# Optimization experiments

Measured on AMD Instinct MI355X. Metric: run time of the kernel, lower is better.

## Reference

```python
import jax, jax.numpy as jnp
import numpy as np

K = 3          # kernel_size
STRIDE = 1
BLOCK = 64     # block_size
OUT_FEATURES = 512
IN_CH = 256
IN_FEATURES = K * K * IN_CH          # 2304
Q = IN_FEATURES // BLOCK             # 36 (exact)
P = OUT_FEATURES // BLOCK            # 8


def _unfold(x, k, stride):
    # torch F.unfold with padding=k//2: output (B, C*k*k, Ho*Wo),
    # feature order channel-major then (di, dj)
    B, C, H, W = x.shape
    pad = k // 2
    xp = jnp.pad(x, ((0, 0), (0, 0), (pad, pad), (pad, pad)))
    Ho = (H + 2 * pad - k) // stride + 1
    Wo = (W + 2 * pad - k) // stride + 1
    cols = jnp.stack(
        [xp[:, :, di:di + (Ho - 1) * stride + 1:stride,
                  dj:dj + (Wo - 1) * stride + 1:stride]
         for di in range(k) for dj in range(k)],
        axis=2)  # (B, C, k*k, Ho, Wo)
    return cols.reshape(B, C * k * k, Ho * Wo), Ho, Wo


def setup_inputs() -> dict:
    key = jax.random.key(0)
    k1, k2 = jax.random.split(key)
    x = jax.random.normal(k1, (8, IN_CH, 32, 32), dtype=jnp.float32)
    # xavier-uniform-like init on (p, q, block)
    fan_in, fan_out = Q * BLOCK, P * BLOCK
    a = float(np.sqrt(6.0 / (fan_in + fan_out)))
    weight = jax.random.uniform(k2, (P, Q, BLOCK), dtype=jnp.float32,
                                minval=-a, maxval=a)
    return {"x": x, "weight": weight}


def reference(x, weight):
    B = x.shape[0]
    H = x.shape[2]
    xu, Ho, Wo = _unfold(x, K, STRIDE)          # (B, in_features, L)
    pad_rows = Q * BLOCK - IN_FEATURES          # 0 here, kept for faithfulness
    xu = jnp.pad(xu, ((0, 0), (0, pad_rows), (0, 0)))
    # faithful to torch reshape semantics (row-major over (B, q*b, L))
    xb = xu.reshape(-1, Q, BLOCK)               # (N, q, b), N = B*L
    xf = jnp.fft.rfft(xb)                       # (N, q, bf)
    wf = jnp.fft.rfft(weight)                   # (p, q, bf)
    hf = jnp.sum(xf[:, None, :, :] * wf[None, :, :, :], axis=2)  # (N, p, bf)
    h = jnp.fft.irfft(hf, n=BLOCK)              # (N, p, b)
    h = h.reshape(-1, P * BLOCK)
    if P * BLOCK > OUT_FEATURES:
        h = h[:, :OUT_FEATURES]
    L = (H // STRIDE) * (H // STRIDE)
    h = h.reshape(B, L, OUT_FEATURES)
    h = jnp.transpose(h, (0, 2, 1))
    return h.reshape(B, OUT_FEATURES, H // STRIDE, H // STRIDE)
```

## Files before the change

### kernel.cpp

```cpp
#include <hip/hip_runtime.h>
#include <hip/hip_bf16.h>


#define QK 2304
#define NOC 512
#define QB 36
#define QB2 18
#define XPLN 1088
#define MROWS_FALLBACK 8192

typedef __attribute__((ext_vector_type(8))) short short8;
typedef __attribute__((ext_vector_type(4))) float floatx4;

__device__ __forceinline__ ushort f2bf(float f) {
    __hip_bfloat16 h = __float2bfloat16(f);
    return *reinterpret_cast<ushort*>(&h);
}

__device__ __forceinline__ void async16(const void* g, void* l) {
    __builtin_amdgcn_global_load_lds((const __attribute__((address_space(1))) void*)g,
                                     (__attribute__((address_space(3))) void*)l, 16, 0, 0);
}

#define PREP_A_BLOCKS 2048
#define PREP_B_BLOCKS 576

__global__ __launch_bounds__(256) void bcc_prep(const float* __restrict__ x,
                                                const float* __restrict__ w,
                                                ushort* __restrict__ wsX,
                                                ushort* __restrict__ wsB) {
    if (blockIdx.x < PREP_A_BLOCKS) {
        __shared__ float img[1024];
        const int bb = blockIdx.x >> 8, c = blockIdx.x & 255;
        const float* src = x + ((size_t)bb * 256 + c) * 1024;
        *(float4*)&img[threadIdx.x * 4] = *(const float4*)&src[threadIdx.x * 4];
        __syncthreads();

        for (int t = threadIdx.x; t < 816; t += 256) {
            const int cp = t / 272;
            const int rem = t - cp * 272;
            const int i = rem >> 3, j0 = (rem & 7) * 4;
            const int srow = i - 1;
            const bool rok = (unsigned)srow < 32u;
            ushort u[4];
            #pragma unroll
            for (int e = 0; e < 4; ++e) {
                int scol = j0 + e + cp - 1;
                float v = (rok && (unsigned)scol < 32u) ? img[srow * 32 + scol] : 0.f;
                u[e] = f2bf(v);
            }
            *(ushort4*)&wsX[((size_t)(cp * 2048 + bb * 256 + c)) * XPLN + i * 32 + j0] =
                make_ushort4(u[0], u[1], u[2], u[3]);
        }
    } else {
        int t = (blockIdx.x - PREP_A_BLOCKS) * 256 + threadIdx.x;
        int n = t / 288;
        int o = t - n * 288;
        int p = n >> 6, tt = n & 63;
        int k0 = o * 8;
        ushort u[8];
        #pragma unroll
        for (int e = 0; e < 8; ++e) {
            int k = k0 + e;
            int q = k >> 6, s = k & 63;
            u[e] = f2bf(w[(p * QB + q) * 64 + ((tt - s) & 63)]);
        }
        *(ushort4*)&wsB[(size_t)n * QK + k0]     = make_ushort4(u[0], u[1], u[2], u[7 - 7]);
        *(ushort4*)&wsB[(size_t)n * QK + k0]     = make_ushort4(u[0], u[1], u[2], u[3]);
        *(ushort4*)&wsB[(size_t)n * QK + k0 + 4] = make_ushort4(u[4], u[5], u[6], u[7]);
    }
}

__global__ __launch_bounds__(512) void bcc_mfma(const ushort* __restrict__ X,
                                                const ushort* __restrict__ Bm,
                                                float* __restrict__ out) {
    __shared__ ushort smem[2][2][16384];

    const int tid = threadIdx.x;
    const int l = tid & 63, w = tid >> 6;
    const int t3 = w & 3, ks = w >> 2;
    const int wm = t3 & 1, wn = t3 >> 1;

    const int lin = blockIdx.x;
    const int n_idx = (lin >> 3) & 3;
    const int m_idx = ((lin >> 5) << 3) | (lin & 7);
    const int n0 = n_idx * 128;
    const int m0 = m_idx * 128;
    const int b  = m0 >> 10, r0 = m0 & 1023;
    const int bc0 = b << 8;

    const int lr = l & 15, lq = l >> 4;
    const int lrow = l >> 3, lch = l & 7;
    const int scl = lch ^ lrow;

    floatx4 acc[4][4];
    #pragma unroll
    for (int i = 0; i < 4; ++i)
        #pragma unroll
        for (int j = 0; j < 4; ++j) acc[i][j] = (floatx4){0.f, 0.f, 0.f, 0.f};

    auto stage = [&](int q, int buf) {
        const int kb = q * 128;
        const int r = r0 + w * 16 + lrow;
        size_t eiA[2];
        #pragma unroll
        for (int h = 0; h < 2; ++h) {
            const int fb = r * QK + kb + h * 64 + scl * 8;
            const int kf = fb >> 10, loc = fb & 1023;
            const int c  = (kf * 7282) >> 16;
            const int k9 = kf - c * 9;
            const int di = (k9 * 11) >> 5;
            const int dj = k9 - di * 3;
            eiA[h] = (size_t)((dj << 11) + bc0 + c) * XPLN
                   + ((loc >> 5) + di) * 32 + (loc & 31);
        }
        const size_t bB = (size_t)(n0 + w * 16 + lrow) * QK + kb + scl * 8;
        #pragma unroll
        for (int gg = 0; gg < 2; ++gg)
            #pragma unroll
            for (int h = 0; h < 2; ++h) {
                const int dst = (w * 2 + gg) * 1024 + h * 512;
                async16(X + eiA[h] + gg * (2 * XPLN), &smem[buf][0][dst]);
                async16(Bm + bB + (size_t)gg * (8 * QK) + h * 64, &smem[buf][1][dst]);
            }
    };

    stage(0, 0);
    for (int q = 0; q < QB2; ++q) {
        const int buf = q & 1;
        __builtin_amdgcn_s_barrier();
        asm volatile("" ::: "memory");
        if (q + 1 < QB2) {
            stage(q + 1, buf ^ 1);
            asm volatile("s_waitcnt vmcnt(8)" ::: "memory");
        } else {
            asm volatile("s_waitcnt vmcnt(0)" ::: "memory");
        }
        __builtin_amdgcn_s_barrier();
        asm volatile("" ::: "memory");

        #pragma unroll
        for (int kk = 0; kk < 2; ++kk) {
            const int ca = ks * 8 + kk * 4 + lq;
            short8 av[4], bv[4];
            #pragma unroll
            for (int i = 0; i < 4; ++i) {
                int Ra = wm * 64 + i * 16 + lr;
                av[i] = *(const short8*)&smem[buf][0][
                    (Ra >> 3) * 1024 + (ca >> 3) * 512 + (Ra & 7) * 64 + ((ca ^ Ra) & 7) * 8];
            }
            #pragma unroll
            for (int j = 0; j < 4; ++j) {
                int Rb = wn * 64 + j * 16 + lr;
                bv[j] = *(const short8*)&smem[buf][1][
                    (Rb >> 3) * 1024 + (ca >> 3) * 512 + (Rb & 7) * 64 + ((ca ^ Rb) & 7) * 8];
            }
            #pragma unroll
            for (int i = 0; i < 4; ++i)
                #pragma unroll
                for (int j = 0; j < 4; ++j)
                    acc[i][j] = __builtin_amdgcn_mfma_f32_16x16x32_bf16(bv[j], av[i], acc[i][j], 0, 0, 0);
        }
        asm volatile("" ::: "memory");
    }

    __syncthreads();
    float* fsm = (float*)&smem[0][0][0];
    if (ks == 1) {
        #pragma unroll
        for (int i = 0; i < 4; ++i)
            #pragma unroll
            for (int j = 0; j < 4; ++j)
                *(floatx4*)&fsm[t3 * 4096 + (i * 4 + j) * 256 + l * 4] = acc[i][j];
    }
    __syncthreads();
    if (ks == 0) {
        #pragma unroll
        for (int i = 0; i < 4; ++i) {
            int rr = r0 + wm * 64 + i * 16 + lr;
            #pragma unroll
            for (int j = 0; j < 4; ++j) {
                floatx4 o4 = *(const floatx4*)&fsm[t3 * 4096 + (i * 4 + j) * 256 + l * 4];
                #pragma unroll
                for (int e = 0; e < 4; ++e) {
                    int oc = n0 + wn * 64 + j * 16 + lq * 4 + e;
                    out[((size_t)b * NOC + oc) * 1024 + rr] = acc[i][j][e] + o4[e];
                }
            }
        }
    }
}

__global__ __launch_bounds__(256) void bcc_gemm_f32(
    const float* __restrict__ x, const float* __restrict__ w,
    float* __restrict__ out) {
    __shared__ float Asf[64][68];
    __shared__ float Wsf[64][68];
    const int tid = threadIdx.x;
    const int tn = tid & 15, tm = tid >> 4;
    const int p = blockIdx.x;
    const int m0 = blockIdx.y * 64;
    const int b = m0 >> 10, r0 = m0 & 1023;
    const float* xb = x + (size_t)b * (256 * 32 * 32);
    float acc[4][4] = {};
    for (int q = 0; q < QB; ++q) {
        #pragma unroll
        for (int i = 0; i < 16; ++i) {
            int idx = i * 256 + tid;
            int s = idx & 63, mm = idx >> 6;
            int flat = (r0 + mm) * QK + q * 64 + s;
            int feat = flat >> 10, loc = flat & 1023;
            int c = feat / 9, kk = feat - c * 9;
            int hi = (loc >> 5) + (kk / 3) - 1;
            int wi = (loc & 31) + (kk % 3) - 1;
            float v = 0.0f;
            if ((unsigned)hi < 32u && (unsigned)wi < 32u)
                v = xb[(c * 32 + hi) * 32 + wi];
            Asf[mm][s] = v;
        }
        const float* wb = w + (p * QB + q) * 64;
        #pragma unroll
        for (int i = 0; i < 16; ++i) {
            int idx = i * 256 + tid;
            int t = idx & 63, s = idx >> 6;
            Wsf[s][t] = wb[(t - s) & 63];
        }
        __syncthreads();
        #pragma unroll
        for (int s0 = 0; s0 < 64; s0 += 4) {
            float4 a4[4], b4[4];
            #pragma unroll
            for (int i2 = 0; i2 < 4; ++i2)
                a4[i2] = *(const float4*)&Asf[tm * 4 + i2][s0];
            #pragma unroll
            for (int ss = 0; ss < 4; ++ss)
                b4[ss] = *(const float4*)&Wsf[s0 + ss][tn * 4];
            #pragma unroll
            for (int i2 = 0; i2 < 4; ++i2) {
                const float* av = (const float*)&a4[i2];
                #pragma unroll
                for (int ss = 0; ss < 4; ++ss) {
                    float a = av[ss];
                    acc[i2][0] += a * b4[ss].x;
                    acc[i2][1] += a * b4[ss].y;
                    acc[i2][2] += a * b4[ss].z;
                    acc[i2][3] += a * b4[ss].w;
                }
            }
        }
        __syncthreads();
    }
    float* outb = out + (size_t)b * NOC * 1024;
    const int r_base = r0 + tm * 4;
    #pragma unroll
    for (int j = 0; j < 4; ++j) {
        int oc = p * 64 + tn * 4 + j;
        float4 v = make_float4(acc[0][j], acc[1][j], acc[2][j], acc[3][j]);
        *(float4*)&outb[(size_t)oc * 1024 + r_base] = v;
    }
}

extern "C" void kernel_launch(void* const* d_in, const int* in_sizes, int n_in,
                              void* d_out, int out_size, void* d_ws, size_t ws_size,
                              hipStream_t stream) {
    const float* x = (const float*)d_in[0];
    const float* w = (const float*)d_in[1];
    float* out = (float*)d_out;

    const size_t bytesX = (size_t)3 * 2048 * XPLN * sizeof(ushort);
    const size_t bytesB = (size_t)NOC * QK * sizeof(ushort);

    if (ws_size >= bytesX + bytesB) {
        ushort* wsX = (ushort*)d_ws;
        ushort* wsB = (ushort*)((char*)d_ws + bytesX);
        bcc_prep<<<PREP_A_BLOCKS + PREP_B_BLOCKS, 256, 0, stream>>>(x, w, wsX, wsB);
        bcc_mfma<<<256, 512, 0, stream>>>(wsX, wsB, out);
    } else {
        bcc_gemm_f32<<<dim3(8, MROWS_FALLBACK / 64), 256, 0, stream>>>(x, w, out);
    }
}
```

Before: 96.04 us.

## Repartition MFMA warps into 4-way K-split with 64x128 per-warp tiles

The work split among the 8 warps of each block changes. Before, each warp owned a 64x64 output tile with a 2-way K split. Now each warp owns a 64x128 tile (acc[4][8]) and the K dimension is split 4 ways, so each warp reuses every A fragment across 8 B fragments and issues fewer LDS reads per MFMA. The cost is double the accumulator registers and a two-stage cross-warp reduction through shared memory with extra barriers, while launch_bounds(512,2) asks for two blocks per CU. A redundant duplicate store in the weight-prep kernel is also removed.

```diff
diff --git a/kernel.cpp b/kernel.cpp
--- a/kernel.cpp
+++ b/kernel.cpp
@@ -65,21 +65,20 @@
             int q = k >> 6, s = k & 63;
             u[e] = f2bf(w[(p * QB + q) * 64 + ((tt - s) & 63)]);
         }
-        *(ushort4*)&wsB[(size_t)n * QK + k0]     = make_ushort4(u[0], u[1], u[2], u[7 - 7]);
         *(ushort4*)&wsB[(size_t)n * QK + k0]     = make_ushort4(u[0], u[1], u[2], u[3]);
         *(ushort4*)&wsB[(size_t)n * QK + k0 + 4] = make_ushort4(u[4], u[5], u[6], u[7]);
     }
 }
 
-__global__ __launch_bounds__(512) void bcc_mfma(const ushort* __restrict__ X,
-                                                const ushort* __restrict__ Bm,
-                                                float* __restrict__ out) {
+__global__ __launch_bounds__(512, 2) void bcc_mfma(const ushort* __restrict__ X,
+                                                   const ushort* __restrict__ Bm,
+                                                   float* __restrict__ out) {
     __shared__ ushort smem[2][2][16384];
 
     const int tid = threadIdx.x;
     const int l = tid & 63, w = tid >> 6;
-    const int t3 = w & 3, ks = w >> 2;
-    const int wm = t3 & 1, wn = t3 >> 1;
+    const int wm  = w & 1;
+    const int ks4 = w >> 1;
 
     const int lin = blockIdx.x;
     const int n_idx = (lin >> 3) & 3;
@@ -93,11 +92,11 @@
     const int lrow = l >> 3, lch = l & 7;
     const int scl = lch ^ lrow;
 
-    floatx4 acc[4][4];
+    floatx4 acc[4][8];
     #pragma unroll
     for (int i = 0; i < 4; ++i)
         #pragma unroll
-        for (int j = 0; j < 4; ++j) acc[i][j] = (floatx4){0.f, 0.f, 0.f, 0.f};
+        for (int j = 0; j < 8; ++j) acc[i][j] = (floatx4){0.f, 0.f, 0.f, 0.f};
 
     auto stage = [&](int q, int buf) {
         const int kb = q * 128;
@@ -126,6 +125,7 @@
     };
 
     stage(0, 0);
+    const int ca = ks4 * 4 + lq;
     for (int q = 0; q < QB2; ++q) {
         const int buf = q & 1;
         __builtin_amdgcn_s_barrier();
@@ -139,51 +139,68 @@
         __builtin_amdgcn_s_barrier();
         asm volatile("" ::: "memory");
 
-        #pragma unroll
-        for (int kk = 0; kk < 2; ++kk) {
-            const int ca = ks * 8 + kk * 4 + lq;
-            short8 av[4], bv[4];
-            #pragma unroll
-            for (int i = 0; i < 4; ++i) {
-                int Ra = wm * 64 + i * 16 + lr;
-                av[i] = *(const short8*)&smem[buf][0][
-                    (Ra >> 3) * 1024 + (ca >> 3) * 512 + (Ra & 7) * 64 + ((ca ^ Ra) & 7) * 8];
-            }
-            #pragma unroll
-            for (int j = 0; j < 4; ++j) {
-                int Rb = wn * 64 + j * 16 + lr;
-                bv[j] = *(const short8*)&smem[buf][1][
-                    (Rb >> 3) * 1024 + (ca >> 3) * 512 + (Rb & 7) * 64 + ((ca ^ Rb) & 7) * 8];
-            }
+        short8 av[4], bv[8];
+        #pragma unroll
+        for (int i = 0; i < 4; ++i) {
+            int Ra = wm * 64 + i * 16 + lr;
+            av[i] = *(const short8*)&smem[buf][0][
+                (Ra >> 3) * 1024 + (ca >> 3) * 512 + (Ra & 7) * 64 + ((ca ^ Ra) & 7) * 8];
+        }
+        #pragma unroll
+        for (int j = 0; j < 8; ++j) {
+            int Rb = j * 16 + lr;
+            bv[j] = *(const short8*)&smem[buf][1][
+                (Rb >> 3) * 1024 + (ca >> 3) * 512 + (Rb & 7) * 64 + ((ca ^ Rb) & 7) * 8];
+        }
+        #pragma unroll
+        for (int j = 0; j < 8; ++j)
             #pragma unroll
             for (int i = 0; i < 4; ++i)
-                #pragma unroll
-                for (int j = 0; j < 4; ++j)
-                    acc[i][j] = __builtin_amdgcn_mfma_f32_16x16x32_bf16(bv[j], av[i], acc[i][j], 0, 0, 0);
-        }
+                acc[i][j] = __builtin_amdgcn_mfma_f32_16x16x32_bf16(bv[j], av[i], acc[i][j], 0, 0, 0);
+
         asm volatile("" ::: "memory");
     }
 
     __syncthreads();
     float* fsm = (float*)&smem[0][0][0];
-    if (ks == 1) {
+    if (ks4 >= 2) {
+        const int reg = (ks4 - 2) * 2 + wm;
         #pragma unroll
         for (int i = 0; i < 4; ++i)
             #pragma unroll
-            for (int j = 0; j < 4; ++j)
-                *(floatx4*)&fsm[t3 * 4096 + (i * 4 + j) * 256 + l * 4] = acc[i][j];
-    }
-    __syncthreads();
-    if (ks == 0) {
+            for (int j = 0; j < 8; ++j)
+                *(floatx4*)&fsm[reg * 8192 + (i * 8 + j) * 256 + l * 4] = acc[i][j];
+    }
+    __syncthreads();
+    if (ks4 < 2) {
+        const int reg = ks4 * 2 + wm;
+        #pragma unroll
+        for (int i = 0; i < 4; ++i)
+            #pragma unroll
+            for (int j = 0; j < 8; ++j) {
+                floatx4 o4 = *(const floatx4*)&fsm[reg * 8192 + (i * 8 + j) * 256 + l * 4];
+                acc[i][j] += o4;
+            }
+    }
+    __syncthreads();
+    if (ks4 == 1) {
+        #pragma unroll
+        for (int i = 0; i < 4; ++i)
+            #pragma unroll
+            for (int j = 0; j < 8; ++j)
+                *(floatx4*)&fsm[wm * 8192 + (i * 8 + j) * 256 + l * 4] = acc[i][j];
+    }
+    __syncthreads();
+    if (ks4 == 0) {
         #pragma unroll
         for (int i = 0; i < 4; ++i) {
             int rr = r0 + wm * 64 + i * 16 + lr;
             #pragma unroll
-            for (int j = 0; j < 4; ++j) {
-                floatx4 o4 = *(const floatx4*)&fsm[t3 * 4096 + (i * 4 + j) * 256 + l * 4];
+            for (int j = 0; j < 8; ++j) {
+                floatx4 o4 = *(const floatx4*)&fsm[wm * 8192 + (i * 8 + j) * 256 + l * 4];
                 #pragma unroll
                 for (int e = 0; e < 4; ++e) {
-                    int oc = n0 + wn * 64 + j * 16 + lq * 4 + e;
+                    int oc = n0 + j * 16 + lq * 4 + e;
                     out[((size_t)b * NOC + oc) * 1024 + rr] = acc[i][j][e] + o4[e];
                 }
             }
```

After: 96.67 us. About the same (+0.7%).
